# Performance work log

Hardware: AMD Instinct MI355X
Metric: run time of the kernel (lower is better)

The kernel has to match this reference:

```python
import jax, jax.numpy as jnp
import numpy as np

TOP_K = 2  # MoEBlock default


def setup_inputs() -> dict:
    key = jax.random.key(0)
    ks = jax.random.split(key, 7)
    B_, S, D, F, E, R = 2, 2048, 1024, 4096, 4, 4
    x  = jax.random.normal(ks[0], (B_, S, D), dtype=jnp.float32)
    Wg = jax.random.normal(ks[1], (E, D), dtype=jnp.float32) * (1.0 / np.sqrt(D))
    bg = jnp.zeros((E,), dtype=jnp.float32)
    Wi = jax.random.normal(ks[2], (F, D), dtype=jnp.float32) * (1.0 / np.sqrt(D))
    Wo = jax.random.normal(ks[3], (D, F), dtype=jnp.float32) * (1.0 / np.sqrt(F))
    A  = jax.random.normal(ks[4], (E, R, D), dtype=jnp.float32) * (1.0 / np.sqrt(D))
    Bm = jax.random.normal(ks[5], (E, F, R), dtype=jnp.float32) * 0.01
    return {"x": x, "Wg": Wg, "bg": bg, "Wi": Wi, "Wo": Wo, "A": A, "B": Bm}


def reference(x, Wg, bg, Wi, Wo, A, B):
    E = Wg.shape[0]
    # ---- Router: softmax gate + top-k ----
    logits = jnp.einsum('bsd,ed->bse', x, Wg) + bg          # [B,S,E]
    scores = jax.nn.softmax(logits, axis=-1)
    topv, topi = jax.lax.top_k(scores, TOP_K)               # [B,S,K]
    # per-token combine weight for each expert (sum of matching top-k probs)
    w = jnp.sum(jax.nn.one_hot(topi, E, dtype=x.dtype) * topv[..., None], axis=-2)  # [B,S,E]
    # ---- Experts: shared frozen FFN + per-expert LoRA (dense, then masked) ----
    base = jnp.einsum('bsd,fd->bsf', x, Wi)                 # shared wi(x), [B,S,F]
    lora_low = jnp.einsum('bsd,erd->bser', x, A)            # [B,S,E,R]
    lora = jnp.einsum('bser,efr->bsef', lora_low, B)        # [B,S,E,F]
    h = jax.nn.relu(base[:, :, None, :] + lora)             # act(wi(x)+lora), [B,S,E,F]
    expert_out = jnp.einsum('bsef,df->bsed', h, Wo)         # wo(.), [B,S,E,D]
    # ---- Combine ----
    out = jnp.einsum('bse,bsed->bsd', w, expert_out)        # [B,S,D]
    return out
```

## Files before the change

### kernel.cpp

```cpp
#include <hip/hip_runtime.h>
#include <stdint.h>

#define BSz 4096
#define Ddim 1024
#define Fdim 4096
#define Edim 4
#define Rdim 4

typedef __attribute__((ext_vector_type(8))) short bf16x8;
typedef __attribute__((ext_vector_type(4))) float f32x4;

__device__ __forceinline__ unsigned short f2bf(float f) {
  union { float f; uint32_t u; } c; c.f = f;
  return (unsigned short)((c.u + 0x7fffu + ((c.u >> 16) & 1u)) >> 16);
}

__global__ __launch_bounds__(256) void zero_f32(float* __restrict__ p, int n4) {
  int i = blockIdx.x * 256 + threadIdx.x;
  if (i < n4) ((float4*)p)[i] = make_float4(0.f, 0.f, 0.f, 0.f);
}

__global__ __launch_bounds__(256) void cvt_kernel(const float* __restrict__ in,
                                                  unsigned short* __restrict__ out,
                                                  int n4) {
  int i = blockIdx.x * 256 + threadIdx.x;
  if (i < n4) {
    float4 v = ((const float4*)in)[i];
    ushort4 o;
    o.x = f2bf(v.x); o.y = f2bf(v.y); o.z = f2bf(v.z); o.w = f2bf(v.w);
    ((ushort4*)out)[i] = o;
  }
}

__global__ __launch_bounds__(256) void router_kernel(const float* __restrict__ x,
                                                     const float* __restrict__ Wg,
                                                     const float* __restrict__ bg,
                                                     const float* __restrict__ Aw,
                                                     float* __restrict__ meta) {
  __shared__ float xs[Ddim];
  __shared__ float dots[Edim + Edim * Rdim];
  const int t = blockIdx.x;
  const float4* xt = (const float4*)(x + (size_t)t * Ddim);
  for (int i = threadIdx.x; i < Ddim / 4; i += 256) ((float4*)xs)[i] = xt[i];
  __syncthreads();
  const int wave = threadIdx.x >> 6, lane = threadIdx.x & 63;
  for (int d = wave * 5; d < wave * 5 + 5; ++d) {
    const float* wrow = (d < Edim) ? (Wg + (size_t)d * Ddim)
                                   : (Aw + (size_t)(d - Edim) * Ddim);
    float s = 0.f;
    for (int i = lane; i < Ddim; i += 64) s += xs[i] * wrow[i];
    for (int off = 32; off; off >>= 1) s += __shfl_down(s, off);
    if (lane == 0) dots[d] = s;
  }
  __syncthreads();
  if (threadIdx.x == 0) {
    float p[Edim];
    float m = -1e30f;
    for (int e = 0; e < Edim; ++e) { p[e] = dots[e] + bg[e]; m = fmaxf(m, p[e]); }
    float sum = 0.f;
    for (int e = 0; e < Edim; ++e) { p[e] = expf(p[e] - m); sum += p[e]; }
    const float inv = 1.f / sum;
    for (int e = 0; e < Edim; ++e) p[e] *= inv;
    int e0 = 0;
    for (int e = 1; e < Edim; ++e) if (p[e] > p[e0]) e0 = e;
    int e1 = (e0 == 0) ? 1 : 0;
    for (int e = 0; e < Edim; ++e) if (e != e0 && p[e] > p[e1]) e1 = e;
    float* mt = meta + (size_t)t * 16;
    mt[0] = (float)e0; mt[1] = (float)e1; mt[2] = p[e0]; mt[3] = p[e1];
    for (int r = 0; r < Rdim; ++r) {
      mt[4 + r] = dots[Edim + e0 * Rdim + r];
      mt[8 + r] = dots[Edim + e1 * Rdim + r];
    }
    mt[12] = 0.f; mt[13] = 0.f; mt[14] = 0.f; mt[15] = 0.f;
  }
}

template <int EPI>
__global__ __launch_bounds__(256, 3)
void gemm97(const unsigned short* __restrict__ Ag,
            const unsigned short* __restrict__ Bg,
            int K, int kslice, int Ncols,
            const float* __restrict__ meta,
            const float* __restrict__ B2,
            unsigned short* __restrict__ outg,
            float* __restrict__ outf) {
  constexpr int BK = 64;
  __shared__ __align__(16) unsigned short sA[128 * BK];
  __shared__ __align__(16) unsigned short sB[128 * BK];

  const int tid = threadIdx.x;
  const int lane = tid & 63;
  const int wave = tid >> 6;
  const int wr = wave >> 1, wc = wave & 1;
  const int l16 = lane & 15, lhi = lane >> 4;

  const int nwg = gridDim.x * gridDim.y;
  const int lin = blockIdx.y * gridDim.x + blockIdx.x;
  const int cpx = nwg >> 3;
  const int swz = (lin & 7) * cpx + (lin >> 3);
  const int bx = swz % gridDim.x, by = swz / gridDim.x;
  const int bm = by * 128, bn = bx * 128;
  const int kbase = blockIdx.z * kslice;
  const int NT = kslice / BK;

  f32x4 acc[4][4] = {};

  const int srow = tid >> 3;
  const int scol = ((tid & 7) ^ (srow & 7)) * 8;
  const int ldst = tid * 8;

  const int xr = l16 & 7;

  for (int kt = 0; kt < NT; ++kt) {
    const int kof = kbase + kt * BK;
#pragma unroll
    for (int rr = 0; rr < 4; ++rr)
      __builtin_amdgcn_global_load_lds(
          (const __attribute__((address_space(1))) void*)(Ag + (size_t)(bm + srow + rr * 32) * K + kof + scol),
          (__attribute__((address_space(3))) void*)(sA + ldst + rr * 2048), 16, 0, 0);
#pragma unroll
    for (int rr = 0; rr < 4; ++rr)
      __builtin_amdgcn_global_load_lds(
          (const __attribute__((address_space(1))) void*)(Bg + (size_t)(bn + srow + rr * 32) * K + kof + scol),
          (__attribute__((address_space(3))) void*)(sB + ldst + rr * 2048), 16, 0, 0);
    __syncthreads();
#pragma unroll
    for (int kk = 0; kk < 2; ++kk) {
      bf16x8 af[4], bfv[4];
#pragma unroll
      for (int i = 0; i < 4; ++i) {
        const int ra = wr * 64 + i * 16 + l16;
        af[i] = *(const bf16x8*)(sA + ra * BK + ((kk * 4 + lhi) ^ xr) * 8);
        const int rb = wc * 64 + i * 16 + l16;
        bfv[i] = *(const bf16x8*)(sB + rb * BK + ((kk * 4 + lhi) ^ xr) * 8);
      }
#pragma unroll
      for (int i = 0; i < 4; ++i)
#pragma unroll
        for (int j = 0; j < 4; ++j)
          acc[i][j] = __builtin_amdgcn_mfma_f32_16x16x32_bf16(af[i], bfv[j], acc[i][j], 0, 0, 0);
    }
    __syncthreads();
  }

  if (EPI == 0) {
    unsigned short* tile = sA;
#pragma unroll
    for (int mi = 0; mi < 4; ++mi) {
#pragma unroll
      for (int r = 0; r < 4; ++r) {
        const int rowl = wr * 64 + mi * 16 + lhi * 4 + r;
        const int row = bm + rowl;
        const float* mt = meta + (size_t)row * 16;
        const int e0 = (int)mt[0], e1 = (int)mt[1];
        const float w0 = mt[2], w1 = mt[3];
        const float4 l0 = *(const float4*)(mt + 4);
        const float4 l1 = *(const float4*)(mt + 8);
        unsigned short* trow = (rowl < 64 ? sA + rowl * 128 : sB + (rowl - 64) * 128);
#pragma unroll
        for (int ni = 0; ni < 4; ++ni) {
          const int coll = wc * 64 + ni * 16 + l16;
          const int f = bn + coll;
          const float4 b0 = *(const float4*)(B2 + ((size_t)e0 * Fdim + f) * Rdim);
          const float4 b1 = *(const float4*)(B2 + ((size_t)e1 * Fdim + f) * Rdim);
          const float a = acc[mi][ni][r];
          const float lora0 = l0.x * b0.x + l0.y * b0.y + l0.z * b0.z + l0.w * b0.w;
          const float lora1 = l1.x * b1.x + l1.y * b1.y + l1.z * b1.z + l1.w * b1.w;
          const float gv = w0 * fmaxf(a + lora0, 0.f) + w1 * fmaxf(a + lora1, 0.f);
          trow[coll] = f2bf(gv);
        }
      }
    }
    __syncthreads();
#pragma unroll
    for (int rnd = 0; rnd < 8; ++rnd) {
      const int idx = rnd * 256 + tid;
      const int rowl = idx >> 4;
      const int chk = idx & 15;
      const unsigned short* src = (rowl < 64 ? sA + rowl * 128 : sB + (rowl - 64) * 128) + chk * 8;
      *(bf16x8*)(outg + (size_t)(bm + rowl) * Fdim + bn + chk * 8) = *(const bf16x8*)src;
    }
  } else {
#pragma unroll
    for (int mi = 0; mi < 4; ++mi)
#pragma unroll
      for (int ni = 0; ni < 4; ++ni)
#pragma unroll
        for (int r = 0; r < 4; ++r) {
          const int row = bm + wr * 64 + mi * 16 + lhi * 4 + r;
          const int col = bn + wc * 64 + ni * 16 + l16;
          unsafeAtomicAdd(&outf[(size_t)row * Ncols + col], acc[mi][ni][r]);
        }
  }
}

extern "C" void kernel_launch(void* const* d_in, const int* in_sizes, int n_in,
                              void* d_out, int out_size, void* d_ws, size_t ws_size,
                              hipStream_t stream) {
  const float* x  = (const float*)d_in[0];
  const float* Wg = (const float*)d_in[1];
  const float* bg = (const float*)d_in[2];
  const float* Wi = (const float*)d_in[3];
  const float* Wo = (const float*)d_in[4];
  const float* Aw = (const float*)d_in[5];
  const float* B2 = (const float*)d_in[6];
  float* out = (float*)d_out;

  unsigned short* xb  = (unsigned short*)d_ws;
  unsigned short* wib = xb  + (size_t)BSz  * Ddim;
  unsigned short* wob = wib + (size_t)Fdim * Ddim;
  unsigned short* g   = wob + (size_t)Ddim * Fdim;
  float* meta = (float*)(g + (size_t)BSz * Fdim);

  zero_f32<<<BSz * Ddim / 4 / 256, 256, 0, stream>>>(out, BSz * Ddim / 4);

  const int n4x = BSz * Ddim / 4;
  cvt_kernel<<<(n4x + 255) / 256, 256, 0, stream>>>(x,  xb,  n4x);
  cvt_kernel<<<(n4x + 255) / 256, 256, 0, stream>>>(Wi, wib, n4x);
  cvt_kernel<<<(n4x + 255) / 256, 256, 0, stream>>>(Wo, wob, n4x);

  router_kernel<<<BSz, 256, 0, stream>>>(x, Wg, bg, Aw, meta);

  gemm97<0><<<dim3(Fdim / 128, BSz / 128, 1), 256, 0, stream>>>(
      xb, wib, Ddim, Ddim, Fdim, meta, B2, g, nullptr);

  gemm97<1><<<dim3(Ddim / 128, BSz / 128, 4), 256, 0, stream>>>(
      g, wob, Fdim, Fdim / 4, Ddim, nullptr, nullptr, nullptr, out);
}
```

Before: 193.3 us.

## Replace LDS-staged GEMM with direct global-to-register MFMA operand loads

Both GEMMs drop LDS staging and load MFMA fragments straight from global memory into registers, with no barriers in the K loop. The first GEMM's epilogue now writes bf16 results straight to global memory instead of through an LDS transpose. The aim is to remove LDS traffic and synchronisation, and occupancy is raised to 4 blocks per CU. The cost is that each wave refetches the same A/B data from L2 with no reuse across waves, the loads are 16-byte strided per lane, and the scattered 2-byte output stores are poorly coalesced.

```diff
diff --git a/kernel.cpp b/kernel.cpp
--- a/kernel.cpp
+++ b/kernel.cpp
@@ -76,18 +76,14 @@
 }
 
 template <int EPI>
-__global__ __launch_bounds__(256, 3)
-void gemm97(const unsigned short* __restrict__ Ag,
-            const unsigned short* __restrict__ Bg,
-            int K, int kslice, int Ncols,
-            const float* __restrict__ meta,
-            const float* __restrict__ B2,
-            unsigned short* __restrict__ outg,
-            float* __restrict__ outf) {
-  constexpr int BK = 64;
-  __shared__ __align__(16) unsigned short sA[128 * BK];
-  __shared__ __align__(16) unsigned short sB[128 * BK];
-
+__global__ __launch_bounds__(256, 4)
+void gemm_direct(const unsigned short* __restrict__ Ag,
+                 const unsigned short* __restrict__ Bg,
+                 int K, int kslice, int Ncols,
+                 const float* __restrict__ meta,
+                 const float* __restrict__ B2,
+                 unsigned short* __restrict__ outg,
+                 float* __restrict__ outf) {
   const int tid = threadIdx.x;
   const int lane = tid & 63;
   const int wave = tid >> 6;
@@ -101,84 +97,49 @@
   const int bx = swz % gridDim.x, by = swz / gridDim.x;
   const int bm = by * 128, bn = bx * 128;
   const int kbase = blockIdx.z * kslice;
-  const int NT = kslice / BK;
 
   f32x4 acc[4][4] = {};
 
-  const int srow = tid >> 3;
-  const int scol = ((tid & 7) ^ (srow & 7)) * 8;
-  const int ldst = tid * 8;
+  const unsigned short* ap = Ag + (size_t)(bm + wr * 64 + l16) * K + kbase + lhi * 8;
+  const unsigned short* bp = Bg + (size_t)(bn + wc * 64 + l16) * K + kbase + lhi * 8;
+  const size_t rs16 = (size_t)16 * K;
 
-  const int xr = l16 & 7;
-
-  for (int kt = 0; kt < NT; ++kt) {
-    const int kof = kbase + kt * BK;
+  for (int k = 0; k < kslice; k += 32) {
+    bf16x8 af[4], bfv[4];
 #pragma unroll
-    for (int rr = 0; rr < 4; ++rr)
-      __builtin_amdgcn_global_load_lds(
-          (const __attribute__((address_space(1))) void*)(Ag + (size_t)(bm + srow + rr * 32) * K + kof + scol),
-          (__attribute__((address_space(3))) void*)(sA + ldst + rr * 2048), 16, 0, 0);
+    for (int i = 0; i < 4; ++i) af[i] = *(const bf16x8*)(ap + i * rs16 + k);
 #pragma unroll
-    for (int rr = 0; rr < 4; ++rr)
-      __builtin_amdgcn_global_load_lds(
-          (const __attribute__((address_space(1))) void*)(Bg + (size_t)(bn + srow + rr * 32) * K + kof + scol),
-          (__attribute__((address_space(3))) void*)(sB + ldst + rr * 2048), 16, 0, 0);
-    __syncthreads();
+    for (int j = 0; j < 4; ++j) bfv[j] = *(const bf16x8*)(bp + j * rs16 + k);
 #pragma unroll
-    for (int kk = 0; kk < 2; ++kk) {
-      bf16x8 af[4], bfv[4];
+    for (int i = 0; i < 4; ++i)
 #pragma unroll
-      for (int i = 0; i < 4; ++i) {
-        const int ra = wr * 64 + i * 16 + l16;
-        af[i] = *(const bf16x8*)(sA + ra * BK + ((kk * 4 + lhi) ^ xr) * 8);
-        const int rb = wc * 64 + i * 16 + l16;
-        bfv[i] = *(const bf16x8*)(sB + rb * BK + ((kk * 4 + lhi) ^ xr) * 8);
-      }
-#pragma unroll
-      for (int i = 0; i < 4; ++i)
-#pragma unroll
-        for (int j = 0; j < 4; ++j)
-          acc[i][j] = __builtin_amdgcn_mfma_f32_16x16x32_bf16(af[i], bfv[j], acc[i][j], 0, 0, 0);
-    }
-    __syncthreads();
+      for (int j = 0; j < 4; ++j)
+        acc[i][j] = __builtin_amdgcn_mfma_f32_16x16x32_bf16(af[i], bfv[j], acc[i][j], 0, 0, 0);
   }
 
   if (EPI == 0) {
-    unsigned short* tile = sA;
 #pragma unroll
     for (int mi = 0; mi < 4; ++mi) {
 #pragma unroll
       for (int r = 0; r < 4; ++r) {
-        const int rowl = wr * 64 + mi * 16 + lhi * 4 + r;
-        const int row = bm + rowl;
+        const int row = bm + wr * 64 + mi * 16 + lhi * 4 + r;
         const float* mt = meta + (size_t)row * 16;
         const int e0 = (int)mt[0], e1 = (int)mt[1];
         const float w0 = mt[2], w1 = mt[3];
         const float4 l0 = *(const float4*)(mt + 4);
         const float4 l1 = *(const float4*)(mt + 8);
-        unsigned short* trow = (rowl < 64 ? sA + rowl * 128 : sB + (rowl - 64) * 128);
 #pragma unroll
         for (int ni = 0; ni < 4; ++ni) {
-          const int coll = wc * 64 + ni * 16 + l16;
-          const int f = bn + coll;
+          const int f = bn + wc * 64 + ni * 16 + l16;
           const float4 b0 = *(const float4*)(B2 + ((size_t)e0 * Fdim + f) * Rdim);
           const float4 b1 = *(const float4*)(B2 + ((size_t)e1 * Fdim + f) * Rdim);
           const float a = acc[mi][ni][r];
           const float lora0 = l0.x * b0.x + l0.y * b0.y + l0.z * b0.z + l0.w * b0.w;
           const float lora1 = l1.x * b1.x + l1.y * b1.y + l1.z * b1.z + l1.w * b1.w;
           const float gv = w0 * fmaxf(a + lora0, 0.f) + w1 * fmaxf(a + lora1, 0.f);
-          trow[coll] = f2bf(gv);
+          outg[(size_t)row * Fdim + f] = f2bf(gv);
         }
       }
-    }
-    __syncthreads();
-#pragma unroll
-    for (int rnd = 0; rnd < 8; ++rnd) {
-      const int idx = rnd * 256 + tid;
-      const int rowl = idx >> 4;
-      const int chk = idx & 15;
-      const unsigned short* src = (rowl < 64 ? sA + rowl * 128 : sB + (rowl - 64) * 128) + chk * 8;
-      *(bf16x8*)(outg + (size_t)(bm + rowl) * Fdim + bn + chk * 8) = *(const bf16x8*)src;
     }
   } else {
 #pragma unroll
@@ -221,9 +182,9 @@
 
   router_kernel<<<BSz, 256, 0, stream>>>(x, Wg, bg, Aw, meta);
 
-  gemm97<0><<<dim3(Fdim / 128, BSz / 128, 1), 256, 0, stream>>>(
+  gemm_direct<0><<<dim3(Fdim / 128, BSz / 128, 1), 256, 0, stream>>>(
       xb, wib, Ddim, Ddim, Fdim, meta, B2, g, nullptr);
 
-  gemm97<1><<<dim3(Ddim / 128, BSz / 128, 4), 256, 0, stream>>>(
+  gemm_direct<1><<<dim3(Ddim / 128, BSz / 128, 4), 256, 0, stream>>>(
       g, wob, Fdim, Fdim / 4, Ddim, nullptr, nullptr, nullptr, out);
 }
```

New measurement: 364.3 us. 88.5% more time.
